# Kernel optimization log

Hardware: AMD Instinct MI355X
Metric: run time of the kernel (lower is better)

Reference implementation:

```python
import jax, jax.numpy as jnp
import numpy as np

B, N, C, H = 8, 1024, 768, 12
D = C // H  # 64


def setup_inputs() -> dict:
    key = jax.random.key(0)
    ks = jax.random.split(key, 6)
    x = jax.random.normal(ks[0], (B, N, C), dtype=jnp.float32)
    pad_mask = jnp.ones((B, N), dtype=jnp.int32)
    # params (torch Linear stored transposed; here kept as (in, out) for x @ W)
    s = 1.0 / np.sqrt(C)
    w_attn = jax.random.uniform(ks[1], (C, 3 * C), jnp.float32, -s, s)
    b_attn = jax.random.uniform(ks[2], (3 * C,), jnp.float32, -s, s)
    w_proj = jax.random.uniform(ks[3], (C, C), jnp.float32, -s, s)
    b_proj = jax.random.uniform(ks[4], (C,), jnp.float32, -s, s)
    return {"x": x, "pad_mask": pad_mask, "w_attn": w_attn,
            "b_attn": b_attn, "w_proj": w_proj, "b_proj": b_proj}


def reference(x, pad_mask, w_attn, b_attn, w_proj, b_proj):
    # qkv projection
    qkv = x @ w_attn + b_attn                      # [B,N,3C]
    q, k, v = jnp.split(qkv, 3, axis=-1)
    q = q.reshape(B, N, H, D).transpose(0, 2, 1, 3)  # [B,H,N,D]
    k = k.reshape(B, N, H, D).transpose(0, 2, 1, 3)
    v = v.reshape(B, N, H, D).transpose(0, 2, 1, 3)
    scale = 1.0 / np.sqrt(D)
    att = jnp.einsum('bhqd,bhkd->bhqk', q, k) * scale  # [B,H,N,N]
    # NOTE: original code's causal masked_fill is non-in-place and discarded,
    # so the causal mask is NOT applied. Only the pad mask (over query rows) is.
    pm = pad_mask.reshape(B, 1, N, 1)
    att = jnp.where(pm == 0, -jnp.inf, att)
    att = jax.nn.softmax(att, axis=-1)
    out = jnp.einsum('bhqk,bhkd->bhqd', att, v)     # [B,H,N,D]
    out = out.transpose(0, 2, 1, 3).reshape(B, N, C)
    # dropout layers are identity in eval mode
    return out @ w_proj + b_proj
```

## Files before the change

kernel.cpp:

```cpp
#include <hip/hip_runtime.h>
#include <hip/hip_bf16.h>

#define B_  8
#define N_  1024
#define C_  768
#define H_  12
#define D_  64
#define C3  2304
#define C2  1536

typedef unsigned short ushort_t;
typedef __attribute__((ext_vector_type(8))) short bf16x8;
typedef __attribute__((ext_vector_type(4))) float f32x4;
typedef __attribute__((ext_vector_type(4))) unsigned int u32x4;

__device__ __forceinline__ ushort_t f2bf(float f) {
    union { float f; unsigned int i; } v;
    v.f = f;
    unsigned int x = v.i;
    if ((x & 0x7f800000u) == 0x7f800000u && (x & 0x007fffffu))
        return (ushort_t)((x >> 16) | 0x0040u);
    return (ushort_t)((x + 0x7fffu + ((x >> 16) & 1u)) >> 16);
}

__device__ __forceinline__ void st1(float* p, float v) { *p = v; }
__device__ __forceinline__ void st1(ushort_t* p, float v) { *p = f2bf(v); }

#define NCVT 6144
#define NTA  1728
#define NTP  576

__device__ __forceinline__ void transpose_tile(
    const float* __restrict__ W, ushort_t* __restrict__ WT,
    int K, int Nn, int n0, int k0, float (*t)[33], int tid)
{
    const int tx = tid & 31, ty = tid >> 5;
    #pragma unroll
    for (int i = 0; i < 4; ++i) {
        const int k = ty + i * 8;
        t[k][tx] = W[(size_t)(k0 + k) * Nn + n0 + tx];
    }
    __syncthreads();
    #pragma unroll
    for (int i = 0; i < 4; ++i) {
        const int n = ty + i * 8;
        WT[(size_t)(n0 + n) * K + k0 + tx] = f2bf(t[tx][n]);
    }
}

__global__ __launch_bounds__(256) void prep(
    const float* __restrict__ X, ushort_t* __restrict__ Y,
    const float* __restrict__ Wa, ushort_t* __restrict__ WaT,
    const float* __restrict__ Wp, ushort_t* __restrict__ WpT)
{
    __shared__ float t[32][33];
    const int bid = blockIdx.x;
    const int tid = threadIdx.x;
    if (bid < NCVT) {
        const int i = (bid * 256 + tid) * 4;
        float4 f = *reinterpret_cast<const float4*>(X + i);
        ushort4 o;
        o.x = f2bf(f.x); o.y = f2bf(f.y); o.z = f2bf(f.z); o.w = f2bf(f.w);
        *reinterpret_cast<ushort4*>(Y + i) = o;
    } else if (bid < NCVT + NTA) {
        const int tt = bid - NCVT;
        transpose_tile(Wa, WaT, C_, C3, (tt % (C3 / 32)) * 32,
                       (tt / (C3 / 32)) * 32, t, tid);
    } else {
        const int tt = bid - NCVT - NTA;
        transpose_tile(Wp, WpT, C_, C_, (tt % (C_ / 32)) * 32,
                       (tt / (C_ / 32)) * 32, t, tid);
    }
}

#define GBK 64

__device__ __forceinline__ void gld_lds16(const ushort_t* g, ushort_t* lds) {
    __builtin_amdgcn_global_load_lds(
        (const __attribute__((address_space(1))) void*)g,
        (__attribute__((address_space(3))) void*)lds, 16, 0, 0);
}

template<typename TO, bool SCALEQ>
__global__ __launch_bounds__(256) void gemm_mfma(
    const ushort_t* __restrict__ A, const ushort_t* __restrict__ BT,
    const float* __restrict__ bias, TO* __restrict__ Y, int ldY,
    ushort_t* __restrict__ vtOut, int M, int K, int Nn)
{
    __shared__ ushort_t AB[2][2 * 128 * GBK];

    const int tid  = threadIdx.x;
    const int wave = tid >> 6;
    const int lane = tid & 63;

    const int nbx  = Nn / 128;
    const int nblk = nbx * (M / 128);
    const int hwid = blockIdx.y * gridDim.x + blockIdx.x;
    const int wid  = (hwid & 7) * (nblk >> 3) + (hwid >> 3);
    const int row0 = (wid / nbx) * 128;
    const int col0 = (wid % nbx) * 128;

    const int wr   = (wave >> 1) * 64;
    const int wc   = (wave & 1) * 64;
    const int l15  = lane & 15;
    const int quad = lane >> 4;
    const int l7   = l15 & 7;

    const int srow = lane >> 3;
    const int sg   = (lane & 7) ^ srow;

    f32x4 acc[4][4] = {};

    #pragma unroll
    for (int it = 0; it < 4; ++it) {
        const int baseRow = wave * 32 + it * 8;
        const int r = baseRow + srow;
        gld_lds16(&A [(size_t)(row0 + r) * K + sg * 8], &AB[0][baseRow * GBK]);
        gld_lds16(&BT[(size_t)(col0 + r) * K + sg * 8],
                  &AB[0][128 * GBK + baseRow * GBK]);
    }
    __syncthreads();

    const int nsteps = K / GBK;
    for (int t = 0; t < nsteps; ++t) {
        const int buf = t & 1;
        const ushort_t* const As = AB[buf];
        const ushort_t* const Bs = AB[buf] + 128 * GBK;

        if (t + 1 < nsteps) {
            const int k0 = (t + 1) * GBK;
            #pragma unroll
            for (int it = 0; it < 4; ++it) {
                const int baseRow = wave * 32 + it * 8;
                const int r = baseRow + srow;
                gld_lds16(&A [(size_t)(row0 + r) * K + k0 + sg * 8],
                          &AB[buf ^ 1][baseRow * GBK]);
                gld_lds16(&BT[(size_t)(col0 + r) * K + k0 + sg * 8],
                          &AB[buf ^ 1][128 * GBK + baseRow * GBK]);
            }
        }

        #pragma unroll
        for (int kc = 0; kc < 2; ++kc) {
            bf16x8 af[4], bf[4];
            #pragma unroll
            for (int i = 0; i < 4; ++i) {
                const int aslot = (kc * 4 + quad) ^ l7;
                af[i] = *reinterpret_cast<const bf16x8*>(
                    &As[(wr + i * 16 + l15) * GBK + aslot * 8]);
                bf[i] = *reinterpret_cast<const bf16x8*>(
                    &Bs[(wc + i * 16 + l15) * GBK + aslot * 8]);
            }
            #pragma unroll
            for (int i = 0; i < 4; ++i)
                #pragma unroll
                for (int j = 0; j < 4; ++j)
                    acc[i][j] = __builtin_amdgcn_mfma_f32_16x16x32_bf16(
                        af[i], bf[j], acc[i][j], 0, 0, 0);
        }
        __syncthreads();
    }

    const float qs = (SCALEQ && (col0 + wc) < C_) ? 0.1803368801f : 1.0f;

    if (vtOut != nullptr && col0 >= C2) {
        #pragma unroll
        for (int i = 0; i < 4; ++i) {
            const int r0 = row0 + wr + i * 16 + quad * 4;
            const int bb = r0 >> 10;
            const int n  = r0 & 1023;
            const int np = (n & 0x3E0) | (quad << 3) | ((i & 1) << 2);
            #pragma unroll
            for (int j = 0; j < 4; ++j) {
                const int c  = col0 + wc + j * 16 + l15;
                const int cv = c - C2;
                const int hh = cv >> 6, d = cv & 63;
                const float bv = bias[c];
                ushort4 o;
                o.x = f2bf(acc[i][j][0] + bv);
                o.y = f2bf(acc[i][j][1] + bv);
                o.z = f2bf(acc[i][j][2] + bv);
                o.w = f2bf(acc[i][j][3] + bv);
                *reinterpret_cast<ushort4*>(
                    &vtOut[((size_t)(bb * H_ + hh) * D_ + d) * N_ + np]) = o;
            }
        }
    } else {
        #pragma unroll
        for (int i = 0; i < 4; ++i) {
            const int r = row0 + wr + i * 16 + quad * 4;
            #pragma unroll
            for (int j = 0; j < 4; ++j) {
                const int c = col0 + wc + j * 16 + l15;
                const float bv = bias[c];
                #pragma unroll
                for (int t = 0; t < 4; ++t)
                    st1(&Y[(size_t)(r + t) * ldY + c], (acc[i][j][t] + bv) * qs);
            }
        }
    }
}

__global__ __launch_bounds__(256) void attn_mfma(
    const ushort_t* __restrict__ qk, const ushort_t* __restrict__ vt,
    const int* __restrict__ pad_mask, ushort_t* __restrict__ y)
{
    __shared__ __align__(16) ushort_t KV[2][2 * 64 * 64];

    const int tid  = threadIdx.x;
    const int wave = tid >> 6;
    const int lane = tid & 63;
    const int l15  = lane & 15;
    const int quad = lane >> 4;
    const int l7   = l15 & 7;

    const int wid = (blockIdx.x & 7) * 96 + (blockIdx.x >> 3);
    const int qt = wid & 7;
    const int hb = wid >> 3;
    const int h  = hb % H_;
    const int b  = hb / H_;
    const int q0 = qt * 128 + wave * 32;

    const ushort_t* qkB = qk + (size_t)b * N_ * C2;
    const ushort_t* vtB = vt + ((size_t)(b * H_ + h)) * D_ * N_;
    const int ho = h * D_;

    bf16x8 qf[2][2];
    #pragma unroll
    for (int rt = 0; rt < 2; ++rt)
        #pragma unroll
        for (int kc = 0; kc < 2; ++kc)
            qf[rt][kc] = *reinterpret_cast<const bf16x8*>(
                &qkB[(size_t)(q0 + rt * 16 + l15) * C2 + ho + kc * 32 + quad * 8]);

    int mrow[2][4];
    #pragma unroll
    for (int rt = 0; rt < 2; ++rt)
        #pragma unroll
        for (int t = 0; t < 4; ++t)
            mrow[rt][t] = pad_mask[b * N_ + q0 + rt * 16 + quad * 4 + t];

    f32x4 oacc[2][4] = {};
    float den[2] = {};

    const int srow = lane >> 3;
    const int sg   = (lane & 7) ^ srow;

    #pragma unroll
    for (int it = 0; it < 2; ++it) {
        const int base = wave * 16 + it * 8;
        const int r = base + srow;
        gld_lds16(&qkB[(size_t)r * C2 + C_ + ho + sg * 8], &KV[0][base * 64]);
        gld_lds16(&vtB[(size_t)r * N_ + sg * 8], &KV[0][4096 + base * 64]);
    }
    __syncthreads();

    for (int t = 0; t < N_ / 64; ++t) {
        const int buf = t & 1;
        const ushort_t* const Ks  = KV[buf];
        const ushort_t* const Vts = KV[buf] + 4096;

        if (t + 1 < N_ / 64) {
            const int k0 = (t + 1) * 64;
            #pragma unroll
            for (int it = 0; it < 2; ++it) {
                const int base = wave * 16 + it * 8;
                const int r = base + srow;
                gld_lds16(&qkB[(size_t)(k0 + r) * C2 + C_ + ho + sg * 8],
                          &KV[buf ^ 1][base * 64]);
                gld_lds16(&vtB[(size_t)r * N_ + k0 + sg * 8],
                          &KV[buf ^ 1][4096 + base * 64]);
            }
        }

        f32x4 s[2][4] = {};
        #pragma unroll
        for (int kc = 0; kc < 2; ++kc) {
            bf16x8 kf[4];
            #pragma unroll
            for (int ct = 0; ct < 4; ++ct) {
                const int slot = (kc * 4 + quad) ^ l7;
                kf[ct] = *reinterpret_cast<const bf16x8*>(
                    &Ks[(ct * 16 + l15) * 64 + slot * 8]);
            }
            __builtin_amdgcn_s_setprio(1);
            #pragma unroll
            for (int rt = 0; rt < 2; ++rt)
                #pragma unroll
                for (int ct = 0; ct < 4; ++ct)
                    s[rt][ct] = __builtin_amdgcn_mfma_f32_16x16x32_bf16(
                        kf[ct], qf[rt][kc], s[rt][ct], 0, 0, 0);
            __builtin_amdgcn_s_setprio(0);
        }

        unsigned pk[2][4][2];
        #pragma unroll
        for (int rt = 0; rt < 2; ++rt)
            #pragma unroll
            for (int ct = 0; ct < 4; ++ct) {
                const float p0 = __builtin_amdgcn_exp2f(s[rt][ct][0]);
                const float p1 = __builtin_amdgcn_exp2f(s[rt][ct][1]);
                const float p2 = __builtin_amdgcn_exp2f(s[rt][ct][2]);
                const float p3 = __builtin_amdgcn_exp2f(s[rt][ct][3]);
                den[rt] += (p0 + p1) + (p2 + p3);
                const unsigned x0 = __float_as_uint(p0) + 0x8000u;
                const unsigned x1 = __float_as_uint(p1) + 0x8000u;
                const unsigned x2 = __float_as_uint(p2) + 0x8000u;
                const unsigned x3 = __float_as_uint(p3) + 0x8000u;
                pk[rt][ct][0] = (x0 >> 16) | (x1 & 0xffff0000u);
                pk[rt][ct][1] = (x2 >> 16) | (x3 & 0xffff0000u);
            }

        #pragma unroll
        for (int kc = 0; kc < 2; ++kc) {
            bf16x8 pf[2], vf[4];
            #pragma unroll
            for (int rt = 0; rt < 2; ++rt) {
                const u32x4 pw = (u32x4){pk[rt][kc * 2][0], pk[rt][kc * 2][1],
                                         pk[rt][kc * 2 + 1][0],
                                         pk[rt][kc * 2 + 1][1]};
                pf[rt] = __builtin_bit_cast(bf16x8, pw);
            }
            #pragma unroll
            for (int dt = 0; dt < 4; ++dt) {
                const int slot = (kc * 4 + quad) ^ l7;
                vf[dt] = *reinterpret_cast<const bf16x8*>(
                    &Vts[(dt * 16 + l15) * 64 + slot * 8]);
            }
            __builtin_amdgcn_s_setprio(1);
            #pragma unroll
            for (int rt = 0; rt < 2; ++rt)
                #pragma unroll
                for (int dt = 0; dt < 4; ++dt)
                    oacc[rt][dt] = __builtin_amdgcn_mfma_f32_16x16x32_bf16(
                        pf[rt], vf[dt], oacc[rt][dt], 0, 0, 0);
            __builtin_amdgcn_s_setprio(0);
        }
        __syncthreads();
    }

    ushort_t* const scratch = KV[0] + wave * 32 * 64;

    #pragma unroll
    for (int rt = 0; rt < 2; ++rt) {
        float v = den[rt];
        v += __shfl_xor(v, 16);
        v += __shfl_xor(v, 32);
        den[rt] = v;
    }
    #pragma unroll
    for (int rt = 0; rt < 2; ++rt)
        #pragma unroll
        for (int t = 0; t < 4; ++t) {
            const float dv  = __shfl(den[rt], quad * 4 + t);
            const float inv = mrow[rt][t] ? 1.0f / dv : __builtin_nanf("");
            const int row = rt * 16 + quad * 4 + t;
            #pragma unroll
            for (int dt = 0; dt < 4; ++dt) {
                const int slot = (dt * 2 + (l15 >> 3)) ^ (row & 7);
                scratch[row * 64 + slot * 8 + l7] =
                    f2bf(oacc[rt][dt][t] * inv);
            }
        }
    __syncthreads();
    {
        const int orow = lane >> 1;
        const int og   = (lane & 1) * 4;
        const size_t gr = (size_t)(b * N_ + q0 + orow) * C_ + ho;
        #pragma unroll
        for (int i2 = 0; i2 < 4; ++i2) {
            const int g = og + i2;
            uint4 w = *reinterpret_cast<const uint4*>(
                &scratch[orow * 64 + (g ^ (orow & 7)) * 8]);
            *reinterpret_cast<uint4*>(&y[gr + g * 8]) = w;
        }
    }
}

extern "C" void kernel_launch(void* const* d_in, const int* in_sizes, int n_in,
                              void* d_out, int out_size, void* d_ws, size_t ws_size,
                              hipStream_t stream)
{
    const float* x      = (const float*)d_in[0];
    const int*   pad    = (const int*)d_in[1];
    const float* w_attn = (const float*)d_in[2];
    const float* b_attn = (const float*)d_in[3];
    const float* w_proj = (const float*)d_in[4];
    const float* b_proj = (const float*)d_in[5];
    float* out = (float*)d_out;

    ushort_t* qkb = (ushort_t*)d_ws;
    ushort_t* vtb = qkb + (size_t)B_ * N_ * C2;
    ushort_t* y   = vtb + (size_t)B_ * H_ * D_ * N_;
    ushort_t* xb  = y;
    ushort_t* wat = y + (size_t)B_ * N_ * C_;
    ushort_t* wpt = wat + (size_t)C3 * C_;

    const int M = B_ * N_;

    prep<<<dim3(NCVT + NTA + NTP), dim3(256), 0, stream>>>(
        x, xb, w_attn, wat, w_proj, wpt);

    gemm_mfma<ushort_t, true><<<dim3(C3 / 128, M / 128), dim3(256), 0, stream>>>(
        xb, wat, b_attn, qkb, C2, vtb, M, C_, C3);

    attn_mfma<<<dim3(B_ * H_ * 8), dim3(256), 0, stream>>>(qkb, vtb, pad, y);

    gemm_mfma<float, false><<<dim3(C_ / 128, M / 128), dim3(256), 0, stream>>>(
        y, wpt, b_proj, out, C_, nullptr, M, C_, C_);
}
```

Baseline: 193.6 us.

## Single-buffer attention K/V LDS and compute softmax denominator with MFMA

New measurement: 200.5 us. 1.04x slower.

```diff
diff --git a/kernel.cpp b/kernel.cpp
--- a/kernel.cpp
+++ b/kernel.cpp
@@ -205,7 +205,9 @@
     const ushort_t* __restrict__ qk, const ushort_t* __restrict__ vt,
     const int* __restrict__ pad_mask, ushort_t* __restrict__ y)
 {
-    __shared__ __align__(16) ushort_t KV[2][2 * 64 * 64];
+    __shared__ __align__(16) ushort_t KV[2 * 64 * 64];
+    ushort_t* const Ks  = KV;
+    ushort_t* const Vts = KV + 64 * 64;
 
     const int tid  = threadIdx.x;
     const int wave = tid >> 6;
@@ -241,37 +243,26 @@
             mrow[rt][t] = pad_mask[b * N_ + q0 + rt * 16 + quad * 4 + t];
 
     f32x4 oacc[2][4] = {};
-    float den[2] = {};
+    f32x4 dacc[2] = {};
+    const unsigned onew = 0x3F803F80u;
+    const bf16x8 ones = __builtin_bit_cast(
+        bf16x8, (u32x4){onew, onew, onew, onew});
 
     const int srow = lane >> 3;
     const int sg   = (lane & 7) ^ srow;
 
-    #pragma unroll
-    for (int it = 0; it < 2; ++it) {
-        const int base = wave * 16 + it * 8;
-        const int r = base + srow;
-        gld_lds16(&qkB[(size_t)r * C2 + C_ + ho + sg * 8], &KV[0][base * 64]);
-        gld_lds16(&vtB[(size_t)r * N_ + sg * 8], &KV[0][4096 + base * 64]);
-    }
-    __syncthreads();
-
-    for (int t = 0; t < N_ / 64; ++t) {
-        const int buf = t & 1;
-        const ushort_t* const Ks  = KV[buf];
-        const ushort_t* const Vts = KV[buf] + 4096;
-
-        if (t + 1 < N_ / 64) {
-            const int k0 = (t + 1) * 64;
-            #pragma unroll
-            for (int it = 0; it < 2; ++it) {
-                const int base = wave * 16 + it * 8;
-                const int r = base + srow;
-                gld_lds16(&qkB[(size_t)(k0 + r) * C2 + C_ + ho + sg * 8],
-                          &KV[buf ^ 1][base * 64]);
-                gld_lds16(&vtB[(size_t)r * N_ + k0 + sg * 8],
-                          &KV[buf ^ 1][4096 + base * 64]);
-            }
-        }
+    for (int k0 = 0; k0 < N_; k0 += 64) {
+        __syncthreads();
+        #pragma unroll
+        for (int it = 0; it < 2; ++it) {
+            const int base = wave * 16 + it * 8;
+            const int r = base + srow;
+            gld_lds16(&qkB[(size_t)(k0 + r) * C2 + C_ + ho + sg * 8],
+                      &Ks[base * 64]);
+            gld_lds16(&vtB[(size_t)r * N_ + k0 + sg * 8],
+                      &Vts[base * 64]);
+        }
+        __syncthreads();
 
         f32x4 s[2][4] = {};
         #pragma unroll
@@ -298,17 +289,16 @@
         for (int rt = 0; rt < 2; ++rt)
             #pragma unroll
             for (int ct = 0; ct < 4; ++ct) {
-                const float p0 = __builtin_amdgcn_exp2f(s[rt][ct][0]);
-                const float p1 = __builtin_amdgcn_exp2f(s[rt][ct][1]);
-                const float p2 = __builtin_amdgcn_exp2f(s[rt][ct][2]);
-                const float p3 = __builtin_amdgcn_exp2f(s[rt][ct][3]);
-                den[rt] += (p0 + p1) + (p2 + p3);
-                const unsigned x0 = __float_as_uint(p0) + 0x8000u;
-                const unsigned x1 = __float_as_uint(p1) + 0x8000u;
-                const unsigned x2 = __float_as_uint(p2) + 0x8000u;
-                const unsigned x3 = __float_as_uint(p3) + 0x8000u;
-                pk[rt][ct][0] = (x0 >> 16) | (x1 & 0xffff0000u);
-                pk[rt][ct][1] = (x2 >> 16) | (x3 & 0xffff0000u);
+                const unsigned x0 = __float_as_uint(
+                    __builtin_amdgcn_exp2f(s[rt][ct][0])) + 0x8000u;
+                const unsigned x1 = __float_as_uint(
+                    __builtin_amdgcn_exp2f(s[rt][ct][1])) + 0x8000u;
+                const unsigned x2 = __float_as_uint(
+                    __builtin_amdgcn_exp2f(s[rt][ct][2])) + 0x8000u;
+                const unsigned x3 = __float_as_uint(
+                    __builtin_amdgcn_exp2f(s[rt][ct][3])) + 0x8000u;
+                pk[rt][ct][0] = __builtin_amdgcn_perm(x1, x0, 0x07060302u);
+                pk[rt][ct][1] = __builtin_amdgcn_perm(x3, x2, 0x07060302u);
             }
 
         #pragma unroll
@@ -329,31 +319,27 @@
             }
             __builtin_amdgcn_s_setprio(1);
             #pragma unroll
-            for (int rt = 0; rt < 2; ++rt)
+            for (int rt = 0; rt < 2; ++rt) {
+                dacc[rt] = __builtin_amdgcn_mfma_f32_16x16x32_bf16(
+                    pf[rt], ones, dacc[rt], 0, 0, 0);
                 #pragma unroll
                 for (int dt = 0; dt < 4; ++dt)
                     oacc[rt][dt] = __builtin_amdgcn_mfma_f32_16x16x32_bf16(
                         pf[rt], vf[dt], oacc[rt][dt], 0, 0, 0);
+            }
             __builtin_amdgcn_s_setprio(0);
         }
-        __syncthreads();
-    }
-
-    ushort_t* const scratch = KV[0] + wave * 32 * 64;
-
-    #pragma unroll
-    for (int rt = 0; rt < 2; ++rt) {
-        float v = den[rt];
-        v += __shfl_xor(v, 16);
-        v += __shfl_xor(v, 32);
-        den[rt] = v;
-    }
+    }
+
+    __syncthreads();
+    ushort_t* const scratch = KV + wave * 32 * 64;
+
     #pragma unroll
     for (int rt = 0; rt < 2; ++rt)
         #pragma unroll
         for (int t = 0; t < 4; ++t) {
-            const float dv  = __shfl(den[rt], quad * 4 + t);
-            const float inv = mrow[rt][t] ? 1.0f / dv : __builtin_nanf("");
+            const float inv = mrow[rt][t] ? 1.0f / dacc[rt][t]
+                                          : __builtin_nanf("");
             const int row = rt * 16 + quad * 4 + t;
             #pragma unroll
             for (int dt = 0; dt < 4; ++dt) {
```

## Specialize QKV GEMM with 256x128 tiles, 512 threads, triple-buffered LDS pipeline

Applied to the files above, without the earlier changes.

Result: faster. 188.0 us, median of 2 (-2.9%).

```diff
diff --git a/kernel.cpp b/kernel.cpp
--- a/kernel.cpp
+++ b/kernel.cpp
@@ -81,24 +81,26 @@
         (__attribute__((address_space(3))) void*)lds, 16, 0, 0);
 }
 
-template<typename TO, bool SCALEQ>
-__global__ __launch_bounds__(256) void gemm_mfma(
+#define G1_NBX   18
+#define G1_NBLK  576
+#define G1_STEPS 12
+#define G1_BUFSZ 24576
+
+__global__ __launch_bounds__(512) void gemm1_mfma(
     const ushort_t* __restrict__ A, const ushort_t* __restrict__ BT,
-    const float* __restrict__ bias, TO* __restrict__ Y, int ldY,
-    ushort_t* __restrict__ vtOut, int M, int K, int Nn)
+    const float* __restrict__ bias, ushort_t* __restrict__ Y,
+    ushort_t* __restrict__ vtOut)
 {
-    __shared__ ushort_t AB[2][2 * 128 * GBK];
+    extern __shared__ ushort_t LDSbuf[];
 
     const int tid  = threadIdx.x;
     const int wave = tid >> 6;
     const int lane = tid & 63;
 
-    const int nbx  = Nn / 128;
-    const int nblk = nbx * (M / 128);
-    const int hwid = blockIdx.y * gridDim.x + blockIdx.x;
-    const int wid  = (hwid & 7) * (nblk >> 3) + (hwid >> 3);
-    const int row0 = (wid / nbx) * 128;
-    const int col0 = (wid % nbx) * 128;
+    const int hwid = blockIdx.x;
+    const int wid  = (hwid & 7) * (G1_NBLK >> 3) + (hwid >> 3);
+    const int row0 = (wid / G1_NBX) * 256;
+    const int col0 = (wid % G1_NBX) * 128;
 
     const int wr   = (wave >> 1) * 64;
     const int wc   = (wave & 1) * 64;
@@ -111,34 +113,33 @@
 
     f32x4 acc[4][4] = {};
 
-    #pragma unroll
-    for (int it = 0; it < 4; ++it) {
-        const int baseRow = wave * 32 + it * 8;
-        const int r = baseRow + srow;
-        gld_lds16(&A [(size_t)(row0 + r) * K + sg * 8], &AB[0][baseRow * GBK]);
-        gld_lds16(&BT[(size_t)(col0 + r) * K + sg * 8],
-                  &AB[0][128 * GBK + baseRow * GBK]);
-    }
-    __syncthreads();
-
-    const int nsteps = K / GBK;
-    for (int t = 0; t < nsteps; ++t) {
-        const int buf = t & 1;
-        const ushort_t* const As = AB[buf];
-        const ushort_t* const Bs = AB[buf] + 128 * GBK;
-
-        if (t + 1 < nsteps) {
-            const int k0 = (t + 1) * GBK;
-            #pragma unroll
-            for (int it = 0; it < 4; ++it) {
-                const int baseRow = wave * 32 + it * 8;
-                const int r = baseRow + srow;
-                gld_lds16(&A [(size_t)(row0 + r) * K + k0 + sg * 8],
-                          &AB[buf ^ 1][baseRow * GBK]);
-                gld_lds16(&BT[(size_t)(col0 + r) * K + k0 + sg * 8],
-                          &AB[buf ^ 1][128 * GBK + baseRow * GBK]);
-            }
-        }
+    auto stage = [&](int buf, int k0) {
+        ushort_t* lds = LDSbuf + buf * G1_BUFSZ;
+        #pragma unroll
+        for (int it = 0; it < 4; ++it) {
+            const int baseRow = it * 64 + wave * 8;
+            gld_lds16(&A[(size_t)(row0 + baseRow + srow) * C_ + k0 + sg * 8],
+                      &lds[baseRow * 64]);
+        }
+        #pragma unroll
+        for (int it = 0; it < 2; ++it) {
+            const int baseRow = it * 64 + wave * 8;
+            gld_lds16(&BT[(size_t)(col0 + baseRow + srow) * C_ + k0 + sg * 8],
+                      &lds[16384 + baseRow * 64]);
+        }
+    };
+
+    stage(0, 0);
+    stage(1, GBK);
+    asm volatile("s_waitcnt vmcnt(6)" ::: "memory");
+    __builtin_amdgcn_s_barrier();
+    __builtin_amdgcn_sched_barrier(0);
+
+    for (int t = 0; t < G1_STEPS; ++t) {
+        const ushort_t* const As = LDSbuf + (t % 3) * G1_BUFSZ;
+        const ushort_t* const Bs = As + 16384;
+
+        if (t + 2 < G1_STEPS) stage((t + 2) % 3, (t + 2) * GBK);
 
         #pragma unroll
         for (int kc = 0; kc < 2; ++kc) {
@@ -147,9 +148,9 @@
             for (int i = 0; i < 4; ++i) {
                 const int aslot = (kc * 4 + quad) ^ l7;
                 af[i] = *reinterpret_cast<const bf16x8*>(
-                    &As[(wr + i * 16 + l15) * GBK + aslot * 8]);
+                    &As[(wr + i * 16 + l15) * 64 + aslot * 8]);
                 bf[i] = *reinterpret_cast<const bf16x8*>(
-                    &Bs[(wc + i * 16 + l15) * GBK + aslot * 8]);
+                    &Bs[(wc + i * 16 + l15) * 64 + aslot * 8]);
             }
             #pragma unroll
             for (int i = 0; i < 4; ++i)
@@ -158,12 +159,18 @@
                     acc[i][j] = __builtin_amdgcn_mfma_f32_16x16x32_bf16(
                         af[i], bf[j], acc[i][j], 0, 0, 0);
         }
-        __syncthreads();
-    }
-
-    const float qs = (SCALEQ && (col0 + wc) < C_) ? 0.1803368801f : 1.0f;
-
-    if (vtOut != nullptr && col0 >= C2) {
+
+        if (t + 2 < G1_STEPS)
+            asm volatile("s_waitcnt vmcnt(6)" ::: "memory");
+        else if (t + 1 < G1_STEPS)
+            asm volatile("s_waitcnt vmcnt(0)" ::: "memory");
+        __builtin_amdgcn_s_barrier();
+        __builtin_amdgcn_sched_barrier(0);
+    }
+
+    const float qs = ((col0 + wc) < C_) ? 0.1803368801f : 1.0f;
+
+    if (col0 >= C2) {
         #pragma unroll
         for (int i = 0; i < 4; ++i) {
             const int r0 = row0 + wr + i * 16 + quad * 4;
@@ -195,6 +202,126 @@
                 const float bv = bias[c];
                 #pragma unroll
                 for (int t = 0; t < 4; ++t)
+                    Y[(size_t)(r + t) * C2 + c] = f2bf((acc[i][j][t] + bv) * qs);
+            }
+        }
+    }
+}
+
+template<typename TO, bool SCALEQ>
+__global__ __launch_bounds__(256) void gemm_mfma(
+    const ushort_t* __restrict__ A, const ushort_t* __restrict__ BT,
+    const float* __restrict__ bias, TO* __restrict__ Y, int ldY,
+    ushort_t* __restrict__ vtOut, int M, int K, int Nn)
+{
+    __shared__ ushort_t AB[2][2 * 128 * GBK];
+
+    const int tid  = threadIdx.x;
+    const int wave = tid >> 6;
+    const int lane = tid & 63;
+
+    const int nbx  = Nn / 128;
+    const int nblk = nbx * (M / 128);
+    const int hwid = blockIdx.y * gridDim.x + blockIdx.x;
+    const int wid  = (hwid & 7) * (nblk >> 3) + (hwid >> 3);
+    const int row0 = (wid / nbx) * 128;
+    const int col0 = (wid % nbx) * 128;
+
+    const int wr   = (wave >> 1) * 64;
+    const int wc   = (wave & 1) * 64;
+    const int l15  = lane & 15;
+    const int quad = lane >> 4;
+    const int l7   = l15 & 7;
+
+    const int srow = lane >> 3;
+    const int sg   = (lane & 7) ^ srow;
+
+    f32x4 acc[4][4] = {};
+
+    #pragma unroll
+    for (int it = 0; it < 4; ++it) {
+        const int baseRow = wave * 32 + it * 8;
+        const int r = baseRow + srow;
+        gld_lds16(&A [(size_t)(row0 + r) * K + sg * 8], &AB[0][baseRow * GBK]);
+        gld_lds16(&BT[(size_t)(col0 + r) * K + sg * 8],
+                  &AB[0][128 * GBK + baseRow * GBK]);
+    }
+    __syncthreads();
+
+    const int nsteps = K / GBK;
+    for (int t = 0; t < nsteps; ++t) {
+        const int buf = t & 1;
+        const ushort_t* const As = AB[buf];
+        const ushort_t* const Bs = AB[buf] + 128 * GBK;
+
+        if (t + 1 < nsteps) {
+            const int k0 = (t + 1) * GBK;
+            #pragma unroll
+            for (int it = 0; it < 4; ++it) {
+                const int baseRow = wave * 32 + it * 8;
+                const int r = baseRow + srow;
+                gld_lds16(&A [(size_t)(row0 + r) * K + k0 + sg * 8],
+                          &AB[buf ^ 1][baseRow * GBK]);
+                gld_lds16(&BT[(size_t)(col0 + r) * K + k0 + sg * 8],
+                          &AB[buf ^ 1][128 * GBK + baseRow * GBK]);
+            }
+        }
+
+        #pragma unroll
+        for (int kc = 0; kc < 2; ++kc) {
+            bf16x8 af[4], bf[4];
+            #pragma unroll
+            for (int i = 0; i < 4; ++i) {
+                const int aslot = (kc * 4 + quad) ^ l7;
+                af[i] = *reinterpret_cast<const bf16x8*>(
+                    &As[(wr + i * 16 + l15) * GBK + aslot * 8]);
+                bf[i] = *reinterpret_cast<const bf16x8*>(
+                    &Bs[(wc + i * 16 + l15) * GBK + aslot * 8]);
+            }
+            #pragma unroll
+            for (int i = 0; i < 4; ++i)
+                #pragma unroll
+                for (int j = 0; j < 4; ++j)
+                    acc[i][j] = __builtin_amdgcn_mfma_f32_16x16x32_bf16(
+                        af[i], bf[j], acc[i][j], 0, 0, 0);
+        }
+        __syncthreads();
+    }
+
+    const float qs = (SCALEQ && (col0 + wc) < C_) ? 0.1803368801f : 1.0f;
+
+    if (vtOut != nullptr && col0 >= C2) {
+        #pragma unroll
+        for (int i = 0; i < 4; ++i) {
+            const int r0 = row0 + wr + i * 16 + quad * 4;
+            const int bb = r0 >> 10;
+            const int n  = r0 & 1023;
+            const int np = (n & 0x3E0) | (quad << 3) | ((i & 1) << 2);
+            #pragma unroll
+            for (int j = 0; j < 4; ++j) {
+                const int c  = col0 + wc + j * 16 + l15;
+                const int cv = c - C2;
+                const int hh = cv >> 6, d = cv & 63;
+                const float bv = bias[c];
+                ushort4 o;
+                o.x = f2bf(acc[i][j][0] + bv);
+                o.y = f2bf(acc[i][j][1] + bv);
+                o.z = f2bf(acc[i][j][2] + bv);
+                o.w = f2bf(acc[i][j][3] + bv);
+                *reinterpret_cast<ushort4*>(
+                    &vtOut[((size_t)(bb * H_ + hh) * D_ + d) * N_ + np]) = o;
+            }
+        }
+    } else {
+        #pragma unroll
+        for (int i = 0; i < 4; ++i) {
+            const int r = row0 + wr + i * 16 + quad * 4;
+            #pragma unroll
+            for (int j = 0; j < 4; ++j) {
+                const int c = col0 + wc + j * 16 + l15;
+                const float bv = bias[c];
+                #pragma unroll
+                for (int t = 0; t < 4; ++t)
                     st1(&Y[(size_t)(r + t) * ldY + c], (acc[i][j][t] + bv) * qs);
             }
         }
@@ -398,11 +525,19 @@
 
     const int M = B_ * N_;
 
+    static bool attr_set = false;
+    if (!attr_set) {
+        hipFuncSetAttribute(reinterpret_cast<const void*>(&gemm1_mfma),
+                            hipFuncAttributeMaxDynamicSharedMemorySize,
+                            3 * G1_BUFSZ * 2);
+        attr_set = true;
+    }
+
     prep<<<dim3(NCVT + NTA + NTP), dim3(256), 0, stream>>>(
         x, xb, w_attn, wat, w_proj, wpt);
 
-    gemm_mfma<ushort_t, true><<<dim3(C3 / 128, M / 128), dim3(256), 0, stream>>>(
-        xb, wat, b_attn, qkb, C2, vtb, M, C_, C3);
+    gemm1_mfma<<<dim3(G1_NBLK), dim3(512), 3 * G1_BUFSZ * 2, stream>>>(
+        xb, wat, b_attn, qkb, vtb);
 
     attn_mfma<<<dim3(B_ * H_ * 8), dim3(256), 0, stream>>>(qkb, vtb, pad, y);
 
```
